# Optimization experiments

Measured on AMD Instinct MI355X. Metric: run time of the kernel, lower is better.

## Reference

```python
import jax, jax.numpy as jnp
import numpy as np

B, T, D, H = 8, 1024, 1024, 16
HD = D // H
SCALE = HD ** -0.5


def setup_inputs() -> dict:
    key = jax.random.key(0)
    ks = jax.random.split(key, 5)
    s = 0.02
    return {
        "hidden_states": jax.random.normal(ks[0], (B, T, D), jnp.float32),
        "Wq": jax.random.normal(ks[1], (D, D), jnp.float32) * s,
        "bq": jnp.zeros((D,), jnp.float32),
        "Wk": jax.random.normal(ks[2], (D, D), jnp.float32) * s,
        "bk": jnp.zeros((D,), jnp.float32),
        "Wv": jax.random.normal(ks[3], (D, D), jnp.float32) * s,
        "bv": jnp.zeros((D,), jnp.float32),
        "Wo": jax.random.normal(ks[4], (D, D), jnp.float32) * s,
        "bo": jnp.zeros((D,), jnp.float32),
    }


def _split_heads(x):
    # [B, T, D] -> [B, H, T, HD]
    return x.reshape(B, T, H, HD).transpose(0, 2, 1, 3)


def reference(hidden_states, Wq, bq, Wk, bk, Wv, bv, Wo, bo):
    q = _split_heads((hidden_states @ Wq + bq) * SCALE)
    k = _split_heads(hidden_states @ Wk + bk)
    v = _split_heads(hidden_states @ Wv + bv)
    # [B, H, T, T] attention scores
    scores = jnp.einsum("bhqd,bhkd->bhqk", q, k)
    probs = jax.nn.softmax(scores, axis=-1)
    attn = jnp.einsum("bhqk,bhkd->bhqd", probs, v)
    attn = attn.transpose(0, 2, 1, 3).reshape(B, T, D)
    return attn @ Wo + bo
```

## Files before the change

### kernel.cpp

```cpp
#include <hip/hip_runtime.h>

typedef unsigned short u16;
typedef __attribute__((ext_vector_type(4))) float f32x4;
typedef __attribute__((ext_vector_type(8))) __bf16 bf16x8;
typedef __attribute__((ext_vector_type(4))) __bf16 bf16x4;
typedef __attribute__((ext_vector_type(4))) unsigned short u16x4;
typedef __attribute__((ext_vector_type(8))) unsigned short u16x8;

static __device__ __forceinline__ u16 f2bf(float f) {
    union { float f; unsigned u; } v; v.f = f;
    unsigned r = v.u + 0x7FFFu + ((v.u >> 16) & 1u);
    return (u16)(r >> 16);
}

static __device__ __forceinline__ float exp2f_fast(float x) {
    float r; asm("v_exp_f32 %0, %1" : "=v"(r) : "v"(x)); return r;
}

static __device__ __forceinline__ void gload16(const u16* g, u16* l) {
    __builtin_amdgcn_global_load_lds(
        (const __attribute__((address_space(1))) unsigned int*)g,
        (__attribute__((address_space(3))) unsigned int*)l, 16, 0, 0);
}

#define WAIT_BAR() asm volatile("s_waitcnt vmcnt(0)\n\ts_barrier" ::: "memory")

#define SWZ64(row, ec) (((row) * 64) + ((((ec) ^ ((row) & 7))) << 3))

__global__ __launch_bounds__(256) void k_cvt(const float* __restrict__ in, u16* __restrict__ out) {
    size_t i = (size_t)blockIdx.x * 256 + threadIdx.x;
    float4 v = ((const float4*)in)[i];
    u16x4 o; o[0] = f2bf(v.x); o[1] = f2bf(v.y); o[2] = f2bf(v.z); o[3] = f2bf(v.w);
    *(u16x4*)(out + i * 4) = o;
}

__global__ __launch_bounds__(256) void k_wtrans4(
    const float* __restrict__ W0, const float* __restrict__ W1,
    const float* __restrict__ W2, const float* __restrict__ W3,
    u16* __restrict__ T0, u16* __restrict__ T1, u16* __restrict__ T2, u16* __restrict__ T3,
    float s0) {
    const float* W; u16* Tt; float sc;
    switch (blockIdx.z) {
        case 0:  W = W0; Tt = T0; sc = s0;  break;
        case 1:  W = W1; Tt = T1; sc = 1.f; break;
        case 2:  W = W2; Tt = T2; sc = 1.f; break;
        default: W = W3; Tt = T3; sc = 1.f; break;
    }
    __shared__ float tile[32][33];
    int n0 = blockIdx.x * 32, k0 = blockIdx.y * 32;
    int tid = threadIdx.x;
    int r = tid >> 3, c = (tid & 7) * 4;
    float4 v = *(const float4*)(W + (size_t)(k0 + r) * 1024 + n0 + c);
    tile[r][c] = v.x; tile[r][c + 1] = v.y; tile[r][c + 2] = v.z; tile[r][c + 3] = v.w;
    __syncthreads();
    u16x4 o;
    o[0] = f2bf(tile[c][r] * sc);
    o[1] = f2bf(tile[c + 1][r] * sc);
    o[2] = f2bf(tile[c + 2][r] * sc);
    o[3] = f2bf(tile[c + 3][r] * sc);
    *(u16x4*)(Tt + (size_t)(n0 + r) * 1024 + k0 + c) = o;
}

static __device__ __forceinline__ void gemm_step(const u16* As, const u16* Bs,
                                                 int wm, int wn, int fr, int f8,
                                                 f32x4 acc[4][4]) {
    bf16x8 af[4], bf[4];
#pragma unroll
    for (int mt = 0; mt < 4; ++mt) af[mt] = *(const bf16x8*)(&As[(wm + mt * 16 + fr) * 32 + f8]);
#pragma unroll
    for (int nt = 0; nt < 4; ++nt) bf[nt] = *(const bf16x8*)(&Bs[(wn + nt * 16 + fr) * 32 + f8]);
#pragma unroll
    for (int mt = 0; mt < 4; ++mt)
#pragma unroll
        for (int nt = 0; nt < 4; ++nt)
            acc[mt][nt] = __builtin_amdgcn_mfma_f32_16x16x32_bf16(af[mt], bf[nt], acc[mt][nt], 0, 0, 0);
}

#define GEMM_PRELUDE(A_, B_)                                                    \
    const int tid = threadIdx.x;                                                \
    const int l = tid & 63, w = tid >> 6;                                       \
    const int wm = (w >> 1) * 64, wn = (w & 1) * 64;                            \
    const size_t m0 = (size_t)blockIdx.y * 128, n0 = (size_t)blockIdx.x * 128;  \
    const int fr = l & 15, f8 = (l >> 4) * 8, f4 = (l >> 4) * 4;                \
    const int j0 = w * 2;                                                       \
    const int srow0 = j0 * 16 + (l >> 2), srow1 = srow0 + 16;                   \
    const int scol = (l & 3) * 8;                                               \
    const u16* Ag0 = (A_) + (m0 + srow0) * 1024 + scol;                         \
    const u16* Ag1 = (A_) + (m0 + srow1) * 1024 + scol;                         \
    const u16* Bg0 = (B_) + (n0 + srow0) * 1024 + scol;                         \
    const u16* Bg1 = (B_) + (n0 + srow1) * 1024 + scol;                         \
    const int lo0 = j0 * 512 + l * 8, lo1 = (j0 + 1) * 512 + l * 8;

#define GSTAGE(ASB, BSB, kt)            \
    gload16(Ag0 + (kt), (ASB) + lo0);   \
    gload16(Ag1 + (kt), (ASB) + lo1);   \
    gload16(Bg0 + (kt), (BSB) + lo0);   \
    gload16(Bg1 + (kt), (BSB) + lo1)

#define GEMM_MAINLOOP()                                           \
    f32x4 acc[4][4] = {};                                         \
    GSTAGE(As0, Bs0, 0);                                          \
    WAIT_BAR();                                                   \
    for (int kt = 0; kt < 1024; kt += 64) {                       \
        if (kt + 32 < 1024) { GSTAGE(As1, Bs1, kt + 32); }        \
        gemm_step(As0, Bs0, wm, wn, fr, f8, acc);                 \
        WAIT_BAR();                                               \
        if (kt + 64 < 1024) { GSTAGE(As0, Bs0, kt + 64); }        \
        gemm_step(As1, Bs1, wm, wn, fr, f8, acc);                 \
        WAIT_BAR();                                               \
    }

__global__ __launch_bounds__(256) void k_gemm(const u16* __restrict__ A, const u16* __restrict__ Bt,
                                              const float* __restrict__ bias, float bias_scale,
                                              u16* __restrict__ obf, float* __restrict__ of32,
                                              int ldc, int bias_row) {
    __shared__ u16 As0[128 * 32], Bs0[128 * 32];
    __shared__ u16 As1[128 * 32], Bs1[128 * 32];
    GEMM_PRELUDE(A, Bt)
    GEMM_MAINLOOP()
#pragma unroll
    for (int mt = 0; mt < 4; ++mt) {
        float rb_[4];
#pragma unroll
        for (int r = 0; r < 4; ++r)
            rb_[r] = bias_row ? bias[m0 + wm + mt * 16 + f4 + r] * bias_scale : 0.f;
#pragma unroll
        for (int nt = 0; nt < 4; ++nt) {
            const size_t col = n0 + wn + nt * 16 + fr;
            const float cb = bias_row ? 0.f : bias[col] * bias_scale;
#pragma unroll
            for (int r = 0; r < 4; ++r) {
                const size_t row = m0 + wm + mt * 16 + f4 + r;
                const float vv = acc[mt][nt][r] + cb + rb_[r];
                if (of32) of32[row * (size_t)ldc + col] = vv;
                else      obf[row * (size_t)ldc + col] = f2bf(vv);
            }
        }
    }
}

__global__ __launch_bounds__(256) void k_gemmQK(const u16* __restrict__ A, const u16* __restrict__ Wqkt,
                                                const float* __restrict__ bq, const float* __restrict__ bk,
                                                float qscale, u16* __restrict__ Qb, u16* __restrict__ Kb) {
    __shared__ u16 As0[128 * 32], Bs0[128 * 32];
    __shared__ u16 As1[128 * 32], Bs1[128 * 32];
    GEMM_PRELUDE(A, Wqkt)
    GEMM_MAINLOOP()
    const int seg = (int)(n0 >> 10);
    const float* bias = seg ? bk : bq;
    const float bsc = seg ? 1.f : qscale;
    u16* ob = seg ? Kb : Qb;
#pragma unroll
    for (int mt = 0; mt < 4; ++mt)
#pragma unroll
        for (int nt = 0; nt < 4; ++nt) {
            const size_t colm = (n0 + wn + nt * 16 + fr) & 1023;
            const float bb = bias[colm] * bsc;
#pragma unroll
            for (int r = 0; r < 4; ++r) {
                const size_t row = m0 + wm + mt * 16 + f4 + r;
                ob[row * 1024 + colm] = f2bf(acc[mt][nt][r] + bb);
            }
        }
}

static __device__ __forceinline__ void softmax_grp(const f32x4 s[4], f32x4 o[4],
                                                   float& m, float& lsum, bf16x4 p[4]) {
    float mymax = s[0][0];
#pragma unroll
    for (int nt = 0; nt < 4; ++nt)
#pragma unroll
        for (int r = 0; r < 4; ++r) mymax = fmaxf(mymax, s[nt][r]);
    float ps = 0.f;
#pragma unroll
    for (int nt = 0; nt < 4; ++nt)
#pragma unroll
        for (int r = 0; r < 4; ++r) {
            const float pp = exp2f_fast(s[nt][r]);
            ps += pp; p[nt][r] = (__bf16)pp;
        }
    if (__builtin_expect(__any(mymax > 11.0f), 0)) {
        float rm = fmaxf(mymax, __shfl_xor(mymax, 16, 64));
        rm = fmaxf(rm, __shfl_xor(rm, 32, 64));
        const float d = fmaxf(rm, 0.f);
        const float fac = exp2f_fast(-d);
        m += d; lsum *= fac;
#pragma unroll
        for (int mt = 0; mt < 4; ++mt)
#pragma unroll
            for (int r = 0; r < 4; ++r) o[mt][r] *= fac;
        ps = 0.f;
#pragma unroll
        for (int nt = 0; nt < 4; ++nt)
#pragma unroll
            for (int r = 0; r < 4; ++r) {
                const float pp = exp2f_fast(s[nt][r] - d);
                ps += pp; p[nt][r] = (__bf16)pp;
            }
    }
    lsum += ps;
}

static __device__ __forceinline__ void flash_tile(const u16* Ks, const u16* Vs,
                                                  int fr, int gg,
                                                  bf16x8 qA0, bf16x8 qA1, bf16x8 qB0, bf16x8 qB1,
                                                  f32x4 oA[4], f32x4 oB[4],
                                                  float& mA, float& lA, float& mB, float& lB) {
    f32x4 sA[4], sB[4];
    __builtin_amdgcn_s_setprio(1);
#pragma unroll
    for (int nt = 0; nt < 4; ++nt) {
        const int rk = nt * 16 + fr;
        const bf16x8 kf0 = *(const bf16x8*)(&Ks[SWZ64(rk, gg)]);
        const bf16x8 kf1 = *(const bf16x8*)(&Ks[SWZ64(rk, gg + 4)]);
        f32x4 z = {-mA, -mA, -mA, -mA};
        z = __builtin_amdgcn_mfma_f32_16x16x32_bf16(kf0, qA0, z, 0, 0, 0);
        z = __builtin_amdgcn_mfma_f32_16x16x32_bf16(kf1, qA1, z, 0, 0, 0);
        sA[nt] = z;
        f32x4 y = {-mB, -mB, -mB, -mB};
        y = __builtin_amdgcn_mfma_f32_16x16x32_bf16(kf0, qB0, y, 0, 0, 0);
        y = __builtin_amdgcn_mfma_f32_16x16x32_bf16(kf1, qB1, y, 0, 0, 0);
        sB[nt] = y;
    }
    __builtin_amdgcn_s_setprio(0);
    bf16x4 pA[4], pB[4];
    softmax_grp(sA, oA, mA, lA, pA);
    softmax_grp(sB, oB, mB, lB, pB);
    const bf16x8 BA0 = __builtin_shufflevector(pA[0], pA[1], 0, 1, 2, 3, 4, 5, 6, 7);
    const bf16x8 BA1 = __builtin_shufflevector(pA[2], pA[3], 0, 1, 2, 3, 4, 5, 6, 7);
    const bf16x8 BB0 = __builtin_shufflevector(pB[0], pB[1], 0, 1, 2, 3, 4, 5, 6, 7);
    const bf16x8 BB1 = __builtin_shufflevector(pB[2], pB[3], 0, 1, 2, 3, 4, 5, 6, 7);
    const int e0 = gg >> 1, hf = (gg & 1) * 4;
    __builtin_amdgcn_s_setprio(1);
#pragma unroll
    for (int mt = 0; mt < 4; ++mt) {
        const int rv = mt * 16 + fr;
        const int rs = rv & 7, rb = rv * 64;
        const bf16x4 v0 = *(const bf16x4*)(&Vs[rb + (((e0    ) ^ rs) << 3) + hf]);
        const bf16x4 v1 = *(const bf16x4*)(&Vs[rb + (((e0 + 2) ^ rs) << 3) + hf]);
        const bf16x4 v2 = *(const bf16x4*)(&Vs[rb + (((e0 + 4) ^ rs) << 3) + hf]);
        const bf16x4 v3 = *(const bf16x4*)(&Vs[rb + (((e0 + 6) ^ rs) << 3) + hf]);
        const bf16x8 vk0 = __builtin_shufflevector(v0, v1, 0, 1, 2, 3, 4, 5, 6, 7);
        const bf16x8 vk1 = __builtin_shufflevector(v2, v3, 0, 1, 2, 3, 4, 5, 6, 7);
        oA[mt] = __builtin_amdgcn_mfma_f32_16x16x32_bf16(vk0, BA0, oA[mt], 0, 0, 0);
        oA[mt] = __builtin_amdgcn_mfma_f32_16x16x32_bf16(vk1, BA1, oA[mt], 0, 0, 0);
        oB[mt] = __builtin_amdgcn_mfma_f32_16x16x32_bf16(vk0, BB0, oB[mt], 0, 0, 0);
        oB[mt] = __builtin_amdgcn_mfma_f32_16x16x32_bf16(vk1, BB1, oB[mt], 0, 0, 0);
    }
    __builtin_amdgcn_s_setprio(0);
}

__global__ __launch_bounds__(256, 2) void k_flash(const u16* __restrict__ Q, const u16* __restrict__ K,
                                                  const u16* __restrict__ Vt2, u16* __restrict__ O) {
    __shared__ u16 Ks0[64 * 64], Vs0[64 * 64];
    __shared__ u16 Ks1[64 * 64], Vs1[64 * 64];
    const int tid = threadIdx.x;
    const int l = tid & 63, w = tid >> 6;
    const int id = blockIdx.x;
    const int swz = (id & 7) * 128 + (id >> 3);
    const int bh = swz >> 3, qt = swz & 7;
    const int b = bh >> 4, h = bh & 15;
    const int qw = qt * 128 + w * 32;
    const int fr = l & 15, gg = l >> 4, f4 = gg * 4, f8 = gg * 8;

    const u16* qpA = Q + ((size_t)(b * 1024 + qw + fr)) * 1024 + h * 64 + f8;
    const u16* qpB = qpA + 16 * 1024;
    const bf16x8 qA0 = *(const bf16x8*)qpA;
    const bf16x8 qA1 = *(const bf16x8*)(qpA + 32);
    const bf16x8 qB0 = *(const bf16x8*)qpB;
    const bf16x8 qB1 = *(const bf16x8*)(qpB + 32);

    const int jj0 = w * 2, jj1 = w * 2 + 1;
    const int sr0 = jj0 * 8 + (l >> 3), sr1 = jj1 * 8 + (l >> 3);
    const int sc = ((l & 7) ^ (l >> 3)) * 8;
    const u16* kg0 = K + ((size_t)(b * 1024 + sr0)) * 1024 + h * 64 + sc;
    const u16* kg1 = K + ((size_t)(b * 1024 + sr1)) * 1024 + h * 64 + sc;
    const u16* vg0 = Vt2 + ((size_t)(h * 64 + sr0)) * 8192 + b * 1024 + sc;
    const u16* vg1 = Vt2 + ((size_t)(h * 64 + sr1)) * 8192 + b * 1024 + sc;
    const int lk0 = jj0 * 512 + l * 8, lk1 = jj1 * 512 + l * 8;

#define FSTAGE(KSB, VSB, kt)                            \
    gload16(kg0 + (size_t)(kt) * 1024, (KSB) + lk0);    \
    gload16(kg1 + (size_t)(kt) * 1024, (KSB) + lk1);    \
    gload16(vg0 + (kt), (VSB) + lk0);                   \
    gload16(vg1 + (kt), (VSB) + lk1)

    f32x4 oA[4] = {}, oB[4] = {};
    float mA = 0.f, lA = 0.f, mB = 0.f, lB = 0.f;

    FSTAGE(Ks0, Vs0, 0);
    WAIT_BAR();
    for (int kt0 = 0; kt0 < 1024; kt0 += 128) {
        if (kt0 + 64 < 1024) { FSTAGE(Ks1, Vs1, kt0 + 64); }
        flash_tile(Ks0, Vs0, fr, gg, qA0, qA1, qB0, qB1, oA, oB, mA, lA, mB, lB);
        WAIT_BAR();
        if (kt0 + 128 < 1024) { FSTAGE(Ks0, Vs0, kt0 + 128); }
        flash_tile(Ks1, Vs1, fr, gg, qA0, qA1, qB0, qB1, oA, oB, mA, lA, mB, lB);
        WAIT_BAR();
    }
#undef FSTAGE
    lA += __shfl_xor(lA, 16, 64); lA += __shfl_xor(lA, 32, 64);
    lB += __shfl_xor(lB, 16, 64); lB += __shfl_xor(lB, 32, 64);
    const float ivA = 1.0f / lA, ivB = 1.0f / lB;
    u16* opA = O + ((size_t)(b * 1024 + qw + fr)) * 1024 + h * 64;
    u16* opB = opA + 16 * 1024;
#pragma unroll
    for (int mt = 0; mt < 4; ++mt) {
        u16x4 oa, ob;
#pragma unroll
        for (int r = 0; r < 4; ++r) { oa[r] = f2bf(oA[mt][r] * ivA); ob[r] = f2bf(oB[mt][r] * ivB); }
        *(u16x4*)(opA + mt * 16 + f4) = oa;
        *(u16x4*)(opB + mt * 16 + f4) = ob;
    }
}

extern "C" void kernel_launch(void* const* d_in, const int* in_sizes, int n_in,
                              void* d_out, int out_size, void* d_ws, size_t ws_size,
                              hipStream_t stream) {
    (void)in_sizes; (void)n_in; (void)out_size; (void)ws_size;
    const float* hs = (const float*)d_in[0];
    const float* Wq = (const float*)d_in[1];
    const float* bq = (const float*)d_in[2];
    const float* Wk = (const float*)d_in[3];
    const float* bk = (const float*)d_in[4];
    const float* Wv = (const float*)d_in[5];
    const float* bv = (const float*)d_in[6];
    const float* Wo = (const float*)d_in[7];
    const float* bo = (const float*)d_in[8];
    float* out = (float*)d_out;
    char* ws = (char*)d_ws;
    const size_t MB = 1024ull * 1024ull;
    u16* Xb  = (u16*)(ws);
    u16* Wqt = (u16*)(ws + 16 * MB);
    u16* Wkt = (u16*)(ws + 18 * MB);
    u16* Wvt = (u16*)(ws + 20 * MB);
    u16* Wot = (u16*)(ws + 22 * MB);
    u16* Qb  = (u16*)(ws + 24 * MB);
    u16* Kb  = (u16*)(ws + 40 * MB);
    u16* Vt2 = (u16*)(ws + 56 * MB);
    u16* Ob  = Xb;

    const float SCALE_Q = 0.125f * 1.4426950408889634f;

    k_cvt<<<dim3(8192), dim3(256), 0, stream>>>(hs, Xb);
    k_wtrans4<<<dim3(32, 32, 4), dim3(256), 0, stream>>>(Wq, Wk, Wv, Wo, Wqt, Wkt, Wvt, Wot, SCALE_Q);
    k_gemmQK<<<dim3(16, 64), dim3(256), 0, stream>>>(Xb, Wqt, bq, bk, SCALE_Q, Qb, Kb);
    k_gemm<<<dim3(64, 8), dim3(256), 0, stream>>>(Wvt, Xb, bv, 1.0f, Vt2, nullptr, 8192, 1);
    k_flash<<<dim3(1024), dim3(256), 0, stream>>>(Qb, Kb, Vt2, Ob);
    k_gemm<<<dim3(8, 64), dim3(256), 0, stream>>>(Ob, Wot, bo, 1.0f, nullptr, out, 1024, 0);
}
```

Measured before the change: 180.4 us.

## Triple-buffer GEMM LDS stages, swizzle LDS columns, and raise MFMA priority

The GEMM main loop moves from double to triple buffering in LDS. It waits only for the oldest stage (vmcnt(4)) instead of draining all loads before each barrier, so global-to-LDS copies overlap more with MFMA work. The LDS column index is XOR-swizzled on both the store and read sides to reduce bank conflicts on the bf16x8 fragment reads. s_setprio is raised around the MFMA block. The extra stage adds 16KB of LDS per block, which may reduce occupancy.

```diff
diff --git a/kernel.cpp b/kernel.cpp
--- a/kernel.cpp
+++ b/kernel.cpp
@@ -23,6 +23,7 @@
         (__attribute__((address_space(3))) unsigned int*)l, 16, 0, 0);
 }
 
+#define VMK_BAR(N) asm volatile("s_waitcnt vmcnt(" #N ")\n\ts_barrier" ::: "memory")
 #define WAIT_BAR() asm volatile("s_waitcnt vmcnt(0)\n\ts_barrier" ::: "memory")
 
 #define SWZ64(row, ec) (((row) * 64) + ((((ec) ^ ((row) & 7))) << 3))
@@ -62,18 +63,21 @@
 }
 
 static __device__ __forceinline__ void gemm_step(const u16* As, const u16* Bs,
-                                                 int wm, int wn, int fr, int f8,
+                                                 int wm, int wn, int fr, int gg,
                                                  f32x4 acc[4][4]) {
+    const int co = (gg ^ ((fr >> 1) & 3)) * 8;
     bf16x8 af[4], bf[4];
 #pragma unroll
-    for (int mt = 0; mt < 4; ++mt) af[mt] = *(const bf16x8*)(&As[(wm + mt * 16 + fr) * 32 + f8]);
-#pragma unroll
-    for (int nt = 0; nt < 4; ++nt) bf[nt] = *(const bf16x8*)(&Bs[(wn + nt * 16 + fr) * 32 + f8]);
+    for (int mt = 0; mt < 4; ++mt) af[mt] = *(const bf16x8*)(&As[(wm + mt * 16 + fr) * 32 + co]);
+#pragma unroll
+    for (int nt = 0; nt < 4; ++nt) bf[nt] = *(const bf16x8*)(&Bs[(wn + nt * 16 + fr) * 32 + co]);
+    __builtin_amdgcn_s_setprio(1);
 #pragma unroll
     for (int mt = 0; mt < 4; ++mt)
 #pragma unroll
         for (int nt = 0; nt < 4; ++nt)
             acc[mt][nt] = __builtin_amdgcn_mfma_f32_16x16x32_bf16(af[mt], bf[nt], acc[mt][nt], 0, 0, 0);
+    __builtin_amdgcn_s_setprio(0);
 }
 
 #define GEMM_PRELUDE(A_, B_)                                                    \
@@ -81,10 +85,10 @@
     const int l = tid & 63, w = tid >> 6;                                       \
     const int wm = (w >> 1) * 64, wn = (w & 1) * 64;                            \
     const size_t m0 = (size_t)blockIdx.y * 128, n0 = (size_t)blockIdx.x * 128;  \
-    const int fr = l & 15, f8 = (l >> 4) * 8, f4 = (l >> 4) * 4;                \
+    const int fr = l & 15, gg = l >> 4, f4 = (l >> 4) * 4;                      \
     const int j0 = w * 2;                                                       \
     const int srow0 = j0 * 16 + (l >> 2), srow1 = srow0 + 16;                   \
-    const int scol = (l & 3) * 8;                                               \
+    const int scol = ((l & 3) ^ ((l >> 3) & 3)) * 8;   \
     const u16* Ag0 = (A_) + (m0 + srow0) * 1024 + scol;                         \
     const u16* Ag1 = (A_) + (m0 + srow1) * 1024 + scol;                         \
     const u16* Bg0 = (B_) + (n0 + srow0) * 1024 + scol;                         \
@@ -97,18 +101,18 @@
     gload16(Bg0 + (kt), (BSB) + lo0);   \
     gload16(Bg1 + (kt), (BSB) + lo1)
 
-#define GEMM_MAINLOOP()                                           \
-    f32x4 acc[4][4] = {};                                         \
-    GSTAGE(As0, Bs0, 0);                                          \
-    WAIT_BAR();                                                   \
-    for (int kt = 0; kt < 1024; kt += 64) {                       \
-        if (kt + 32 < 1024) { GSTAGE(As1, Bs1, kt + 32); }        \
-        gemm_step(As0, Bs0, wm, wn, fr, f8, acc);                 \
-        WAIT_BAR();                                               \
-        if (kt + 64 < 1024) { GSTAGE(As0, Bs0, kt + 64); }        \
-        gemm_step(As1, Bs1, wm, wn, fr, f8, acc);                 \
-        WAIT_BAR();                                               \
-    }
+#define GEMM_MAINLOOP()                                                       \
+    f32x4 acc[4][4] = {};                                                     \
+    GSTAGE(As0, Bs0, 0);                                                      \
+    GSTAGE(As1, Bs1, 32);                                                     \
+    for (int t = 0; t < 10; ++t) {                                            \
+        const int kt = 64 + t * 96;                                           \
+        VMK_BAR(4); GSTAGE(As2, Bs2, kt);      gemm_step(As0, Bs0, wm, wn, fr, gg, acc); \
+        VMK_BAR(4); GSTAGE(As0, Bs0, kt + 32); gemm_step(As1, Bs1, wm, wn, fr, gg, acc); \
+        VMK_BAR(4); GSTAGE(As1, Bs1, kt + 64); gemm_step(As2, Bs2, wm, wn, fr, gg, acc); \
+    }                                                                         \
+    VMK_BAR(4); gemm_step(As0, Bs0, wm, wn, fr, gg, acc);                     \
+    VMK_BAR(0); gemm_step(As1, Bs1, wm, wn, fr, gg, acc);
 
 __global__ __launch_bounds__(256) void k_gemm(const u16* __restrict__ A, const u16* __restrict__ Bt,
                                               const float* __restrict__ bias, float bias_scale,
@@ -116,6 +120,7 @@
                                               int ldc, int bias_row) {
     __shared__ u16 As0[128 * 32], Bs0[128 * 32];
     __shared__ u16 As1[128 * 32], Bs1[128 * 32];
+    __shared__ u16 As2[128 * 32], Bs2[128 * 32];
     GEMM_PRELUDE(A, Bt)
     GEMM_MAINLOOP()
 #pragma unroll
@@ -144,6 +149,7 @@
                                                 float qscale, u16* __restrict__ Qb, u16* __restrict__ Kb) {
     __shared__ u16 As0[128 * 32], Bs0[128 * 32];
     __shared__ u16 As1[128 * 32], Bs1[128 * 32];
+    __shared__ u16 As2[128 * 32], Bs2[128 * 32];
     GEMM_PRELUDE(A, Wqkt)
     GEMM_MAINLOOP()
     const int seg = (int)(n0 >> 10);
```

Result: faster. 165.4 us (-8.3%).
